# Kernel optimization log

Hardware: AMD Instinct MI355X
Metric: run time of the kernel (lower is better)

## Reference

```python
import jax, jax.numpy as jnp
import numpy as np

B, S, L = 64, 512, 768


def setup_inputs() -> dict:
    key = jax.random.key(0)
    k1, k2 = jax.random.split(key)
    x = jax.random.normal(k1, (B, S, L), dtype=jnp.float32)
    # matches torch uniform_(-0.1, 0.1) init for the probe matrix b
    b = jax.random.uniform(k2, (L, L), minval=-0.1, maxval=0.1, dtype=jnp.float32)
    return {"x": x, "b": b}


def reference(x, b):
    # Original: z[b,i,j,h] = x_i - x_j; h = einsum('gh,bijh', b, z); dist = sum_g h^2
    # Identity: ||b @ (x_i - x_j)||^2 = ||p_i||^2 + ||p_j||^2 - 2 p_i . p_j,  p = x @ b^T
    p = jnp.einsum('gh,bsh->bsg', b, x)          # [B, S, L] projected points
    sq = jnp.sum(p * p, axis=-1)                 # [B, S]  squared norms
    gram = jnp.einsum('bsg,btg->bst', p, p)      # [B, S, S] inner products
    return sq[:, :, None] + sq[:, None, :] - 2.0 * gram  # [B, S, S]
```

## Files before the change

### kernel.cpp

```cpp
#include <hip/hip_runtime.h>
#include <hip/hip_bf16.h>


using bf16x8 = __attribute__((ext_vector_type(8))) __bf16;
using f32x4  = __attribute__((ext_vector_type(4))) float;
using fl4    = __attribute__((ext_vector_type(4))) float;
using u16x4  = __attribute__((ext_vector_type(4))) unsigned short;
using u32x4  = __attribute__((ext_vector_type(4))) unsigned int;

#define NB 64
#define NS 512
#define NL 768

__device__ __forceinline__ unsigned short f2bf(float f) {
  unsigned u = __builtin_bit_cast(unsigned, f);
  u += 0x7FFFu + ((u >> 16) & 1u);
  return (unsigned short)(u >> 16);
}

__device__ __forceinline__ void gload_lds16(const void* g, void* l) {
  __builtin_amdgcn_global_load_lds(
      (const __attribute__((address_space(1))) void*)g,
      (__attribute__((address_space(3))) void*)l, 16, 0, 0);
}

__device__ __forceinline__ bf16x8 cvt_bf8(fl4 a, fl4 b) {
  unsigned r0, r1, r2, r3;
  asm("v_cvt_pk_bf16_f32 %0, %1, %2" : "=v"(r0) : "v"(a[0]), "v"(a[1]));
  asm("v_cvt_pk_bf16_f32 %0, %1, %2" : "=v"(r1) : "v"(a[2]), "v"(a[3]));
  asm("v_cvt_pk_bf16_f32 %0, %1, %2" : "=v"(r2) : "v"(b[0]), "v"(b[1]));
  asm("v_cvt_pk_bf16_f32 %0, %1, %2" : "=v"(r3) : "v"(b[2]), "v"(b[3]));
  u32x4 t = {r0, r1, r2, r3};
  return __builtin_bit_cast(bf16x8, t);
}

#define MEMFENCE asm volatile("" ::: "memory")

__global__ __launch_bounds__(256) void k_cvt_b(const float* __restrict__ b,
                                               unsigned short* __restrict__ bb) {
  const long t = (long)blockIdx.x * 256 + threadIdx.x;
  fl4 v = *(const fl4*)(b + t * 4);
  u16x4 o;
#pragma unroll
  for (int j = 0; j < 4; ++j) o[j] = f2bf(v[j]);
  *(u16x4*)(bb + t * 4) = o;
}

__global__ __launch_bounds__(256) void k_proj(const float* __restrict__ x,
                                              const unsigned short* __restrict__ bb,
                                              unsigned short* __restrict__ p) {
  __shared__ __align__(16) float          smA[3][128 * 32];
  __shared__ __align__(16) unsigned short smB[3][128 * 32];
  const int tid = threadIdx.x;
  const int w = tid >> 6, l = tid & 63;
  const int wg = ((blockIdx.x & 7) * 192) + (blockIdx.x >> 3);
  const int nt = wg % 6, mt = wg / 6;
  const long m0 = (long)mt * 128, n0 = (long)nt * 128;
  const int wr = (w >> 1) * 64, wc = (w & 1) * 64;

  const int arow = tid >> 3;
  const int acol = ((tid & 7) ^ (arow & 7)) * 4;
  const float* gA = x + (m0 + arow) * (long)NL + acol;
  const int brow = tid >> 2;
  const int bcol = ((tid & 3) ^ (brow & 3)) * 8;
  const unsigned short* gB = bb + (n0 + brow) * (long)NL + bcol;

  const int qh = l >> 4, lr = l & 15;
  const int aoff = (wr + lr) * 128;
  const int asw1 = (qh * 32) ^ ((lr & 7) << 4);
  const int asw2 = (qh * 32 + 16) ^ ((lr & 7) << 4);
  const int boff = (wc + lr) * 64 + ((qh ^ (lr & 3)) << 4);

  f32x4 acc[4][4] = {};

#define STAGE_A(k0, buf)                                                     \
  {                                                                          \
    char* d_ = (char*)&smA[buf][0] + w * 1024;                               \
    const float* s_ = gA + (k0);                                             \
    gload_lds16(s_ + 0 * 32 * NL, d_ + 0 * 4096);                            \
    gload_lds16(s_ + 1 * 32 * NL, d_ + 1 * 4096);                            \
    gload_lds16(s_ + 2 * 32 * NL, d_ + 2 * 4096);                            \
    gload_lds16(s_ + 3 * 32 * NL, d_ + 3 * 4096);                            \
  }
#define STAGE_B(k0, buf)                                                     \
  {                                                                          \
    char* d_ = (char*)&smB[buf][0] + w * 1024;                               \
    const unsigned short* s_ = gB + (k0);                                    \
    gload_lds16(s_, d_);                                                     \
    gload_lds16(s_ + 64 * NL, d_ + 4096);                                    \
  }
#define COMPUTE(buf)                                                         \
  {                                                                          \
    const char* A_  = (const char*)&smA[buf][0];                             \
    const char* B_  = (const char*)&smB[buf][0];                             \
    bf16x8 fa[4], fb[4];                                                     \
    _Pragma("unroll")                                                        \
    for (int m = 0; m < 4; ++m) {                                            \
      fl4 a0 = *(const fl4*)(A_ + aoff + m * 2048 + asw1);                   \
      fl4 a1 = *(const fl4*)(A_ + aoff + m * 2048 + asw2);                   \
      fa[m] = cvt_bf8(a0, a1);                                               \
    }                                                                        \
    _Pragma("unroll")                                                        \
    for (int n = 0; n < 4; ++n)                                              \
      fb[n] = *(const bf16x8*)(B_ + boff + n * 1024);                        \
    _Pragma("unroll")                                                        \
    for (int m = 0; m < 4; ++m)                                              \
      _Pragma("unroll")                                                      \
      for (int n = 0; n < 4; ++n)                                            \
        acc[m][n] = __builtin_amdgcn_mfma_f32_16x16x32_bf16(fa[m], fb[n],    \
                                                            acc[m][n], 0, 0, 0); \
  }

  STAGE_A(0, 0)  STAGE_B(0, 0)
  STAGE_A(32, 1) STAGE_B(32, 1)
  int cur = 0, nxt2 = 2;
#pragma unroll 1
  for (int kt = 0; kt < 23; ++kt) {
    asm volatile("s_waitcnt vmcnt(6)" ::: "memory");
    __builtin_amdgcn_s_barrier();
    MEMFENCE;
    if (kt < 22) {
      STAGE_A((kt + 2) * 32, nxt2)
      STAGE_B((kt + 2) * 32, nxt2)
    }
    COMPUTE(cur)
    cur = (cur == 2) ? 0 : cur + 1;
    nxt2 = (nxt2 == 2) ? 0 : nxt2 + 1;
  }
  asm volatile("s_waitcnt vmcnt(0)" ::: "memory");
  __builtin_amdgcn_s_barrier();
  MEMFENCE;
  COMPUTE(cur)
#undef STAGE_A
#undef STAGE_B
#undef COMPUTE

#pragma unroll
  for (int m = 0; m < 4; ++m) {
    const long rbase = m0 + wr + m * 16 + qh * 4;
#pragma unroll
    for (int n = 0; n < 4; ++n) {
      const long col = n0 + wc + n * 16 + lr;
#pragma unroll
      for (int r = 0; r < 4; ++r)
        p[(rbase + r) * NL + col] = f2bf(acc[m][n][r]);
    }
  }
}

__global__ __launch_bounds__(256) void k_sq(const unsigned short* __restrict__ p,
                                            float* __restrict__ sq) {
  const int row = blockIdx.x * 4 + (threadIdx.x >> 6);
  const int l = threadIdx.x & 63;
  const unsigned short* pr = p + (long)row * NL;
  float s = 0.f;
#pragma unroll
  for (int c = 0; c < 3; ++c) {
    u16x4 v = *(const u16x4*)(pr + (c * 64 + l) * 4);
#pragma unroll
    for (int j = 0; j < 4; ++j) {
      float f = __builtin_bit_cast(float, ((unsigned)v[j]) << 16);
      s += f * f;
    }
  }
#pragma unroll
  for (int d = 32; d >= 1; d >>= 1) s += __shfl_xor(s, d, 64);
  if (l == 0) sq[row] = s;
}

__global__ __launch_bounds__(256) void k_gram(const unsigned short* __restrict__ p,
                                              const float* __restrict__ sq,
                                              float* __restrict__ out) {
  __shared__ __align__(16) unsigned short smA[3][128 * 32];
  __shared__ __align__(16) unsigned short smB[3][128 * 32];
  const int tid = threadIdx.x;
  const int w = tid >> 6, l = tid & 63;
  const int wg = ((blockIdx.x & 7) * 128) + (blockIdx.x >> 3);
  const int batch = wg >> 4, tile = wg & 15;
  const int mt = tile >> 2, nt = tile & 3;
  const unsigned short* pb = p + (long)batch * NS * NL;
  const long m0 = (long)mt * 128, n0 = (long)nt * 128;
  const int wr = (w >> 1) * 64, wc = (w & 1) * 64;

  const int srow = tid >> 2;
  const int scol = ((tid & 3) ^ (srow & 3)) * 8;
  const unsigned short* gA = pb + (m0 + srow) * (long)NL + scol;
  const unsigned short* gB = pb + (n0 + srow) * (long)NL + scol;

  const int qh = l >> 4, lr = l & 15;
  const int aoff = (wr + lr) * 64 + ((qh ^ (lr & 3)) << 4);
  const int boff = (wc + lr) * 64 + ((qh ^ (lr & 3)) << 4);

  f32x4 acc[4][4] = {};

#define STAGE2(k0, buf)                                                      \
  {                                                                          \
    char* da_ = (char*)&smA[buf][0] + w * 1024;                              \
    char* db_ = (char*)&smB[buf][0] + w * 1024;                              \
    gload_lds16(gA + (k0), da_);                                             \
    gload_lds16(gA + (k0) + 64 * NL, da_ + 4096);                            \
    gload_lds16(gB + (k0), db_);                                             \
    gload_lds16(gB + (k0) + 64 * NL, db_ + 4096);                            \
  }
#define COMPUTE2(buf)                                                        \
  {                                                                          \
    const char* A_ = (const char*)&smA[buf][0];                              \
    const char* B_ = (const char*)&smB[buf][0];                              \
    bf16x8 fa[4], fb[4];                                                     \
    _Pragma("unroll")                                                        \
    for (int m = 0; m < 4; ++m)                                              \
      fa[m] = *(const bf16x8*)(A_ + aoff + m * 1024);                        \
    _Pragma("unroll")                                                        \
    for (int n = 0; n < 4; ++n)                                              \
      fb[n] = *(const bf16x8*)(B_ + boff + n * 1024);                        \
    _Pragma("unroll")                                                        \
    for (int m = 0; m < 4; ++m)                                              \
      _Pragma("unroll")                                                      \
      for (int n = 0; n < 4; ++n)                                            \
        acc[m][n] = __builtin_amdgcn_mfma_f32_16x16x32_bf16(fa[m], fb[n],    \
                                                            acc[m][n], 0, 0, 0); \
  }

  STAGE2(0, 0)
  STAGE2(32, 1)
  int cur = 0, nxt2 = 2;
#pragma unroll 1
  for (int kt = 0; kt < 23; ++kt) {
    asm volatile("s_waitcnt vmcnt(4)" ::: "memory");
    __builtin_amdgcn_s_barrier();
    MEMFENCE;
    if (kt < 22) STAGE2((kt + 2) * 32, nxt2)
    COMPUTE2(cur)
    cur = (cur == 2) ? 0 : cur + 1;
    nxt2 = (nxt2 == 2) ? 0 : nxt2 + 1;
  }
  asm volatile("s_waitcnt vmcnt(0)" ::: "memory");
  __builtin_amdgcn_s_barrier();
  MEMFENCE;
  COMPUTE2(cur)
#undef STAGE2
#undef COMPUTE2

  const float* sqb = sq + batch * NS;
  float* outb = out + (long)batch * NS * NS;
  float sqc[4];
#pragma unroll
  for (int n = 0; n < 4; ++n) sqc[n] = sqb[n0 + wc + n * 16 + lr];
#pragma unroll
  for (int m = 0; m < 4; ++m) {
#pragma unroll
    for (int r = 0; r < 4; ++r) {
      const long row = m0 + wr + m * 16 + qh * 4 + r;
      const float sr = sqb[row];
#pragma unroll
      for (int n = 0; n < 4; ++n) {
        const long col = n0 + wc + n * 16 + lr;
        outb[row * NS + col] = sr + sqc[n] - 2.0f * acc[m][n][r];
      }
    }
  }
}

extern "C" void kernel_launch(void* const* d_in, const int* in_sizes, int n_in,
                              void* d_out, int out_size, void* d_ws, size_t ws_size,
                              hipStream_t stream) {
  (void)in_sizes; (void)n_in; (void)out_size; (void)ws_size;
  const float* x = (const float*)d_in[0];
  const float* b = (const float*)d_in[1];
  float* out = (float*)d_out;
  char* ws = (char*)d_ws;
  unsigned short* bb = (unsigned short*)ws;
  float* sq          = (float*)(ws + 1179648);
  unsigned short* p  = (unsigned short*)(ws + 1310720);

  k_cvt_b<<<576, 256, 0, stream>>>(b, bb);
  k_proj <<<1536, 256, 0, stream>>>(x, bb, p);
  k_sq   <<<8192, 256, 0, stream>>>(p, sq);
  k_gram <<<1024, 256, 0, stream>>>(p, sq, out);
}
```

Before: 131.8 us.

## Convert x to bf16 once per tile via registers, double-buffer projection LDS

The projection kernel now loads fp32 x tiles into registers, converts each element to bf16 once, and writes bf16 into a padded, swizzled LDS buffer. Previously the fp32 data went straight to LDS via global_load_lds and was converted after every fragment read. The pipeline also shrinks from three LDS stages to two, with a full vmcnt(0) wait and a barrier each iteration. The LDS swizzle for B (and the gram kernel's operands) changes to XOR with (row>>1)&3 to reduce bank conflicts. This halves LDS footprint and traffic for A, but it loses the async direct-to-LDS copy and the deeper prefetch, so more global latency may be exposed.

```diff
diff --git a/kernel.cpp b/kernel.cpp
--- a/kernel.cpp
+++ b/kernel.cpp
@@ -24,16 +24,6 @@
       (__attribute__((address_space(3))) void*)l, 16, 0, 0);
 }
 
-__device__ __forceinline__ bf16x8 cvt_bf8(fl4 a, fl4 b) {
-  unsigned r0, r1, r2, r3;
-  asm("v_cvt_pk_bf16_f32 %0, %1, %2" : "=v"(r0) : "v"(a[0]), "v"(a[1]));
-  asm("v_cvt_pk_bf16_f32 %0, %1, %2" : "=v"(r1) : "v"(a[2]), "v"(a[3]));
-  asm("v_cvt_pk_bf16_f32 %0, %1, %2" : "=v"(r2) : "v"(b[0]), "v"(b[1]));
-  asm("v_cvt_pk_bf16_f32 %0, %1, %2" : "=v"(r3) : "v"(b[2]), "v"(b[3]));
-  u32x4 t = {r0, r1, r2, r3};
-  return __builtin_bit_cast(bf16x8, t);
-}
-
 #define MEMFENCE asm volatile("" ::: "memory")
 
 __global__ __launch_bounds__(256) void k_cvt_b(const float* __restrict__ b,
@@ -49,8 +39,8 @@
 __global__ __launch_bounds__(256) void k_proj(const float* __restrict__ x,
                                               const unsigned short* __restrict__ bb,
                                               unsigned short* __restrict__ p) {
-  __shared__ __align__(16) float          smA[3][128 * 32];
-  __shared__ __align__(16) unsigned short smB[3][128 * 32];
+  __shared__ __align__(16) unsigned short smA[2][128 * 40];
+  __shared__ __align__(16) unsigned short smB[2][128 * 32];
   const int tid = threadIdx.x;
   const int w = tid >> 6, l = tid & 63;
   const int wg = ((blockIdx.x & 7) * 192) + (blockIdx.x >> 3);
@@ -58,51 +48,66 @@
   const long m0 = (long)mt * 128, n0 = (long)nt * 128;
   const int wr = (w >> 1) * 64, wc = (w & 1) * 64;
 
-  const int arow = tid >> 3;
-  const int acol = ((tid & 7) ^ (arow & 7)) * 4;
-  const float* gA = x + (m0 + arow) * (long)NL + acol;
+  const int arow = tid >> 1, ah = tid & 1;
+  const float* gA = x + (m0 + arow) * (long)NL + ah * 16;
+  const int as_ = (arow >> 3) & 3;
+  const int awr0 = arow * 80 + (((2 * ah + 0) ^ as_) << 4);
+  const int awr1 = arow * 80 + (((2 * ah + 1) ^ as_) << 4);
+
   const int brow = tid >> 2;
-  const int bcol = ((tid & 3) ^ (brow & 3)) * 8;
+  const int bcol = ((tid & 3) ^ ((brow >> 1) & 3)) * 8;
   const unsigned short* gB = bb + (n0 + brow) * (long)NL + bcol;
 
   const int qh = l >> 4, lr = l & 15;
-  const int aoff = (wr + lr) * 128;
-  const int asw1 = (qh * 32) ^ ((lr & 7) << 4);
-  const int asw2 = (qh * 32 + 16) ^ ((lr & 7) << 4);
-  const int boff = (wc + lr) * 64 + ((qh ^ (lr & 3)) << 4);
+  int aro[4];
+#pragma unroll
+  for (int m = 0; m < 4; ++m) {
+    const int r = wr + m * 16 + lr;
+    aro[m] = r * 80 + ((qh ^ ((r >> 3) & 3)) << 4);
+  }
+  const int boff = (wc + lr) * 64 + ((qh ^ ((lr >> 1) & 3)) << 4);
 
   f32x4 acc[4][4] = {};
-
-#define STAGE_A(k0, buf)                                                     \
-  {                                                                          \
-    char* d_ = (char*)&smA[buf][0] + w * 1024;                               \
-    const float* s_ = gA + (k0);                                             \
-    gload_lds16(s_ + 0 * 32 * NL, d_ + 0 * 4096);                            \
-    gload_lds16(s_ + 1 * 32 * NL, d_ + 1 * 4096);                            \
-    gload_lds16(s_ + 2 * 32 * NL, d_ + 2 * 4096);                            \
-    gload_lds16(s_ + 3 * 32 * NL, d_ + 3 * 4096);                            \
-  }
-#define STAGE_B(k0, buf)                                                     \
+  fl4 ar0, ar1, ar2, ar3;
+
+#define ISSUE_B(k0, buf)                                                     \
   {                                                                          \
     char* d_ = (char*)&smB[buf][0] + w * 1024;                               \
-    const unsigned short* s_ = gB + (k0);                                    \
-    gload_lds16(s_, d_);                                                     \
-    gload_lds16(s_ + 64 * NL, d_ + 4096);                                    \
+    gload_lds16(gB + (k0), d_);                                              \
+    gload_lds16(gB + (k0) + 64 * NL, d_ + 4096);                             \
+  }
+#define ISSUE_A(k0)                                                          \
+  {                                                                          \
+    ar0 = *(const fl4*)(gA + (k0));                                          \
+    ar1 = *(const fl4*)(gA + (k0) + 4);                                      \
+    ar2 = *(const fl4*)(gA + (k0) + 8);                                      \
+    ar3 = *(const fl4*)(gA + (k0) + 12);                                     \
+  }
+#define WRITE_A(buf)                                                         \
+  {                                                                          \
+    unsigned q0, q1, q2, q3, q4, q5, q6, q7;                                 \
+    asm("v_cvt_pk_bf16_f32 %0, %1, %2" : "=v"(q0) : "v"(ar0[0]), "v"(ar0[1]));\
+    asm("v_cvt_pk_bf16_f32 %0, %1, %2" : "=v"(q1) : "v"(ar0[2]), "v"(ar0[3]));\
+    asm("v_cvt_pk_bf16_f32 %0, %1, %2" : "=v"(q2) : "v"(ar1[0]), "v"(ar1[1]));\
+    asm("v_cvt_pk_bf16_f32 %0, %1, %2" : "=v"(q3) : "v"(ar1[2]), "v"(ar1[3]));\
+    asm("v_cvt_pk_bf16_f32 %0, %1, %2" : "=v"(q4) : "v"(ar2[0]), "v"(ar2[1]));\
+    asm("v_cvt_pk_bf16_f32 %0, %1, %2" : "=v"(q5) : "v"(ar2[2]), "v"(ar2[3]));\
+    asm("v_cvt_pk_bf16_f32 %0, %1, %2" : "=v"(q6) : "v"(ar3[0]), "v"(ar3[1]));\
+    asm("v_cvt_pk_bf16_f32 %0, %1, %2" : "=v"(q7) : "v"(ar3[2]), "v"(ar3[3]));\
+    u32x4 c0 = {q0, q1, q2, q3}, c1 = {q4, q5, q6, q7};                      \
+    char* base_ = (char*)&smA[buf][0];                                       \
+    *(u32x4*)(base_ + awr0) = c0;                                            \
+    *(u32x4*)(base_ + awr1) = c1;                                            \
   }
 #define COMPUTE(buf)                                                         \
   {                                                                          \
-    const char* A_  = (const char*)&smA[buf][0];                             \
-    const char* B_  = (const char*)&smB[buf][0];                             \
+    const char* A_ = (const char*)&smA[buf][0];                              \
+    const char* B_ = (const char*)&smB[buf][0];                              \
     bf16x8 fa[4], fb[4];                                                     \
     _Pragma("unroll")                                                        \
-    for (int m = 0; m < 4; ++m) {                                            \
-      fl4 a0 = *(const fl4*)(A_ + aoff + m * 2048 + asw1);                   \
-      fl4 a1 = *(const fl4*)(A_ + aoff + m * 2048 + asw2);                   \
-      fa[m] = cvt_bf8(a0, a1);                                               \
-    }                                                                        \
-    _Pragma("unroll")                                                        \
-    for (int n = 0; n < 4; ++n)                                              \
-      fb[n] = *(const bf16x8*)(B_ + boff + n * 1024);                        \
+    for (int m = 0; m < 4; ++m) fa[m] = *(const bf16x8*)(A_ + aro[m]);       \
+    _Pragma("unroll")                                                        \
+    for (int n = 0; n < 4; ++n) fb[n] = *(const bf16x8*)(B_ + boff + n * 1024);\
     _Pragma("unroll")                                                        \
     for (int m = 0; m < 4; ++m)                                              \
       _Pragma("unroll")                                                      \
@@ -111,28 +116,33 @@
                                                             acc[m][n], 0, 0, 0); \
   }
 
-  STAGE_A(0, 0)  STAGE_B(0, 0)
-  STAGE_A(32, 1) STAGE_B(32, 1)
-  int cur = 0, nxt2 = 2;
-#pragma unroll 1
-  for (int kt = 0; kt < 23; ++kt) {
-    asm volatile("s_waitcnt vmcnt(6)" ::: "memory");
-    __builtin_amdgcn_s_barrier();
-    MEMFENCE;
-    if (kt < 22) {
-      STAGE_A((kt + 2) * 32, nxt2)
-      STAGE_B((kt + 2) * 32, nxt2)
-    }
-    COMPUTE(cur)
-    cur = (cur == 2) ? 0 : cur + 1;
-    nxt2 = (nxt2 == 2) ? 0 : nxt2 + 1;
-  }
+  ISSUE_B(0, 0)
+  ISSUE_A(0)
   asm volatile("s_waitcnt vmcnt(0)" ::: "memory");
+  WRITE_A(0)
+  asm volatile("s_waitcnt lgkmcnt(0)" ::: "memory");
   __builtin_amdgcn_s_barrier();
   MEMFENCE;
-  COMPUTE(cur)
-#undef STAGE_A
-#undef STAGE_B
+  int cur = 0;
+#pragma unroll 1
+  for (int kt = 0; kt < 24; ++kt) {
+    if (kt < 23) {
+      ISSUE_B((kt + 1) * 32, cur ^ 1)
+      ISSUE_A((kt + 1) * 32)
+    }
+    COMPUTE(cur)
+    if (kt < 23) {
+      asm volatile("s_waitcnt vmcnt(0)" ::: "memory");
+      WRITE_A(cur ^ 1)
+      asm volatile("s_waitcnt lgkmcnt(0)" ::: "memory");
+      __builtin_amdgcn_s_barrier();
+      MEMFENCE;
+      cur ^= 1;
+    }
+  }
+#undef ISSUE_B
+#undef ISSUE_A
+#undef WRITE_A
 #undef COMPUTE
 
 #pragma unroll
@@ -183,13 +193,13 @@
   const int wr = (w >> 1) * 64, wc = (w & 1) * 64;
 
   const int srow = tid >> 2;
-  const int scol = ((tid & 3) ^ (srow & 3)) * 8;
+  const int scol = ((tid & 3) ^ ((srow >> 1) & 3)) * 8;
   const unsigned short* gA = pb + (m0 + srow) * (long)NL + scol;
   const unsigned short* gB = pb + (n0 + srow) * (long)NL + scol;
 
   const int qh = l >> 4, lr = l & 15;
-  const int aoff = (wr + lr) * 64 + ((qh ^ (lr & 3)) << 4);
-  const int boff = (wc + lr) * 64 + ((qh ^ (lr & 3)) << 4);
+  const int aoff = (wr + lr) * 64 + ((qh ^ ((lr >> 1) & 3)) << 4);
+  const int boff = (wc + lr) * 64 + ((qh ^ ((lr >> 1) & 3)) << 4);
 
   f32x4 acc[4][4] = {};
 
```

Result: faster. 120.2 us (-8.8%).

## Pre-convert x to bf16 and widen projection and gram tiles to 128x256

Applied to the files above, without the earlier changes.

Adds a separate pass that converts x to bf16 in workspace, so the projection GEMM streams bf16 for both operands instead of loading fp32 and converting inside the inner loop. Both GEMM kernels move from 128x128 to 128x256 tiles, with 4x8 MFMA accumulators per wave, a new LDS swizzle and launch bounds of 2 blocks. The larger tiles aim to raise operand reuse and cut global and LDS traffic per FLOP. In exchange, the extra pass reads the full fp32 x and writes about 50MB of bf16 through memory, and register pressure and per-block LDS rise while block counts halve.

```diff
diff --git a/kernel.cpp b/kernel.cpp
--- a/kernel.cpp
+++ b/kernel.cpp
@@ -6,7 +6,6 @@
 using f32x4  = __attribute__((ext_vector_type(4))) float;
 using fl4    = __attribute__((ext_vector_type(4))) float;
 using u16x4  = __attribute__((ext_vector_type(4))) unsigned short;
-using u32x4  = __attribute__((ext_vector_type(4))) unsigned int;
 
 #define NB 64
 #define NS 512
@@ -22,16 +21,6 @@
   __builtin_amdgcn_global_load_lds(
       (const __attribute__((address_space(1))) void*)g,
       (__attribute__((address_space(3))) void*)l, 16, 0, 0);
-}
-
-__device__ __forceinline__ bf16x8 cvt_bf8(fl4 a, fl4 b) {
-  unsigned r0, r1, r2, r3;
-  asm("v_cvt_pk_bf16_f32 %0, %1, %2" : "=v"(r0) : "v"(a[0]), "v"(a[1]));
-  asm("v_cvt_pk_bf16_f32 %0, %1, %2" : "=v"(r1) : "v"(a[2]), "v"(a[3]));
-  asm("v_cvt_pk_bf16_f32 %0, %1, %2" : "=v"(r2) : "v"(b[0]), "v"(b[1]));
-  asm("v_cvt_pk_bf16_f32 %0, %1, %2" : "=v"(r3) : "v"(b[2]), "v"(b[3]));
-  u32x4 t = {r0, r1, r2, r3};
-  return __builtin_bit_cast(bf16x8, t);
 }
 
 #define MEMFENCE asm volatile("" ::: "memory")
@@ -46,100 +35,99 @@
   *(u16x4*)(bb + t * 4) = o;
 }
 
-__global__ __launch_bounds__(256) void k_proj(const float* __restrict__ x,
-                                              const unsigned short* __restrict__ bb,
-                                              unsigned short* __restrict__ p) {
-  __shared__ __align__(16) float          smA[3][128 * 32];
-  __shared__ __align__(16) unsigned short smB[3][128 * 32];
+__global__ __launch_bounds__(256) void k_cvt_x(const float* __restrict__ x,
+                                               unsigned short* __restrict__ xb) {
+  const long n4 = (long)NB * NS * NL / 4;
+  const long stride = (long)gridDim.x * 256;
+  for (long i = (long)blockIdx.x * 256 + threadIdx.x; i < n4; i += stride) {
+    fl4 v = *(const fl4*)(x + i * 4);
+    u16x4 o;
+#pragma unroll
+    for (int j = 0; j < 4; ++j) o[j] = f2bf(v[j]);
+    *(u16x4*)(xb + i * 4) = o;
+  }
+}
+
+__global__ __launch_bounds__(256, 2) void k_projb(
+    const unsigned short* __restrict__ xb,
+    const unsigned short* __restrict__ bb,
+    unsigned short* __restrict__ p) {
+  __shared__ __align__(16) unsigned short smA[3][128 * 32];
+  __shared__ __align__(16) unsigned short smB[3][256 * 32];
   const int tid = threadIdx.x;
   const int w = tid >> 6, l = tid & 63;
-  const int wg = ((blockIdx.x & 7) * 192) + (blockIdx.x >> 3);
-  const int nt = wg % 6, mt = wg / 6;
-  const long m0 = (long)mt * 128, n0 = (long)nt * 128;
-  const int wr = (w >> 1) * 64, wc = (w & 1) * 64;
-
-  const int arow = tid >> 3;
-  const int acol = ((tid & 7) ^ (arow & 7)) * 4;
-  const float* gA = x + (m0 + arow) * (long)NL + acol;
-  const int brow = tid >> 2;
-  const int bcol = ((tid & 3) ^ (brow & 3)) * 8;
-  const unsigned short* gB = bb + (n0 + brow) * (long)NL + bcol;
+  const int wg = ((blockIdx.x & 7) * 96) + (blockIdx.x >> 3);
+  const int nt = wg % 3, mt = wg / 3;
+  const long m0 = (long)mt * 128, n0 = (long)nt * 256;
+  const int wr = (w >> 1) * 64, wc = (w & 1) * 128;
+
+  const int srow = tid >> 2;
+  const int scol = ((tid & 3) ^ ((srow >> 1) & 3)) * 8;
+  const unsigned short* gA = xb + (m0 + srow) * (long)NL + scol;
+  const unsigned short* gB = bb + (n0 + srow) * (long)NL + scol;
 
   const int qh = l >> 4, lr = l & 15;
-  const int aoff = (wr + lr) * 128;
-  const int asw1 = (qh * 32) ^ ((lr & 7) << 4);
-  const int asw2 = (qh * 32 + 16) ^ ((lr & 7) << 4);
-  const int boff = (wc + lr) * 64 + ((qh ^ (lr & 3)) << 4);
-
-  f32x4 acc[4][4] = {};
-
-#define STAGE_A(k0, buf)                                                     \
-  {                                                                          \
-    char* d_ = (char*)&smA[buf][0] + w * 1024;                               \
-    const float* s_ = gA + (k0);                                             \
-    gload_lds16(s_ + 0 * 32 * NL, d_ + 0 * 4096);                            \
-    gload_lds16(s_ + 1 * 32 * NL, d_ + 1 * 4096);                            \
-    gload_lds16(s_ + 2 * 32 * NL, d_ + 2 * 4096);                            \
-    gload_lds16(s_ + 3 * 32 * NL, d_ + 3 * 4096);                            \
-  }
-#define STAGE_B(k0, buf)                                                     \
-  {                                                                          \
-    char* d_ = (char*)&smB[buf][0] + w * 1024;                               \
-    const unsigned short* s_ = gB + (k0);                                    \
-    gload_lds16(s_, d_);                                                     \
-    gload_lds16(s_ + 64 * NL, d_ + 4096);                                    \
-  }
-#define COMPUTE(buf)                                                         \
-  {                                                                          \
-    const char* A_  = (const char*)&smA[buf][0];                             \
-    const char* B_  = (const char*)&smB[buf][0];                             \
-    bf16x8 fa[4], fb[4];                                                     \
-    _Pragma("unroll")                                                        \
-    for (int m = 0; m < 4; ++m) {                                            \
-      fl4 a0 = *(const fl4*)(A_ + aoff + m * 2048 + asw1);                   \
-      fl4 a1 = *(const fl4*)(A_ + aoff + m * 2048 + asw2);                   \
-      fa[m] = cvt_bf8(a0, a1);                                               \
-    }                                                                        \
-    _Pragma("unroll")                                                        \
-    for (int n = 0; n < 4; ++n)                                              \
+  const int swz = ((qh ^ ((lr >> 1) & 3)) << 4);
+  const int aoff = (wr + lr) * 64 + swz;
+  const int boff = (wc + lr) * 64 + swz;
+
+  f32x4 acc[4][8] = {};
+
+#define STAGEP(k0, buf)                                                      \
+  {                                                                          \
+    char* da_ = (char*)&smA[buf][0] + w * 1024;                              \
+    char* db_ = (char*)&smB[buf][0] + w * 1024;                              \
+    gload_lds16(gA + (k0), da_);                                             \
+    gload_lds16(gA + (k0) + 64 * NL, da_ + 4096);                            \
+    gload_lds16(gB + (k0), db_);                                             \
+    gload_lds16(gB + (k0) + 64 * NL, db_ + 4096);                            \
+    gload_lds16(gB + (k0) + 128 * NL, db_ + 8192);                           \
+    gload_lds16(gB + (k0) + 192 * NL, db_ + 12288);                          \
+  }
+#define COMPUTEP(buf)                                                        \
+  {                                                                          \
+    const char* A_ = (const char*)&smA[buf][0];                              \
+    const char* B_ = (const char*)&smB[buf][0];                              \
+    bf16x8 fa[4], fb[8];                                                     \
+    _Pragma("unroll")                                                        \
+    for (int m = 0; m < 4; ++m)                                              \
+      fa[m] = *(const bf16x8*)(A_ + aoff + m * 1024);                        \
+    _Pragma("unroll")                                                        \
+    for (int n = 0; n < 8; ++n)                                              \
       fb[n] = *(const bf16x8*)(B_ + boff + n * 1024);                        \
     _Pragma("unroll")                                                        \
     for (int m = 0; m < 4; ++m)                                              \
       _Pragma("unroll")                                                      \
-      for (int n = 0; n < 4; ++n)                                            \
+      for (int n = 0; n < 8; ++n)                                            \
         acc[m][n] = __builtin_amdgcn_mfma_f32_16x16x32_bf16(fa[m], fb[n],    \
                                                             acc[m][n], 0, 0, 0); \
   }
 
-  STAGE_A(0, 0)  STAGE_B(0, 0)
-  STAGE_A(32, 1) STAGE_B(32, 1)
+  STAGEP(0, 0)
+  STAGEP(32, 1)
   int cur = 0, nxt2 = 2;
 #pragma unroll 1
   for (int kt = 0; kt < 23; ++kt) {
     asm volatile("s_waitcnt vmcnt(6)" ::: "memory");
     __builtin_amdgcn_s_barrier();
     MEMFENCE;
-    if (kt < 22) {
-      STAGE_A((kt + 2) * 32, nxt2)
-      STAGE_B((kt + 2) * 32, nxt2)
-    }
-    COMPUTE(cur)
+    if (kt < 22) STAGEP((kt + 2) * 32, nxt2)
+    COMPUTEP(cur)
     cur = (cur == 2) ? 0 : cur + 1;
     nxt2 = (nxt2 == 2) ? 0 : nxt2 + 1;
   }
   asm volatile("s_waitcnt vmcnt(0)" ::: "memory");
   __builtin_amdgcn_s_barrier();
   MEMFENCE;
-  COMPUTE(cur)
-#undef STAGE_A
-#undef STAGE_B
-#undef COMPUTE
+  COMPUTEP(cur)
+#undef STAGEP
+#undef COMPUTEP
 
 #pragma unroll
   for (int m = 0; m < 4; ++m) {
     const long rbase = m0 + wr + m * 16 + qh * 4;
 #pragma unroll
-    for (int n = 0; n < 4; ++n) {
+    for (int n = 0; n < 8; ++n) {
       const long col = n0 + wc + n * 16 + lr;
 #pragma unroll
       for (int r = 0; r < 4; ++r)
@@ -168,32 +156,34 @@
   if (l == 0) sq[row] = s;
 }
 
-__global__ __launch_bounds__(256) void k_gram(const unsigned short* __restrict__ p,
-                                              const float* __restrict__ sq,
-                                              float* __restrict__ out) {
+__global__ __launch_bounds__(256, 2) void k_gram(
+    const unsigned short* __restrict__ p,
+    const float* __restrict__ sq,
+    float* __restrict__ out) {
   __shared__ __align__(16) unsigned short smA[3][128 * 32];
-  __shared__ __align__(16) unsigned short smB[3][128 * 32];
+  __shared__ __align__(16) unsigned short smB[3][256 * 32];
   const int tid = threadIdx.x;
   const int w = tid >> 6, l = tid & 63;
-  const int wg = ((blockIdx.x & 7) * 128) + (blockIdx.x >> 3);
-  const int batch = wg >> 4, tile = wg & 15;
-  const int mt = tile >> 2, nt = tile & 3;
+  const int wg = ((blockIdx.x & 7) * 64) + (blockIdx.x >> 3);
+  const int batch = wg >> 3, tile = wg & 7;
+  const int mt = tile >> 1, nt = tile & 1;
   const unsigned short* pb = p + (long)batch * NS * NL;
-  const long m0 = (long)mt * 128, n0 = (long)nt * 128;
-  const int wr = (w >> 1) * 64, wc = (w & 1) * 64;
+  const long m0 = (long)mt * 128, n0 = (long)nt * 256;
+  const int wr = (w >> 1) * 64, wc = (w & 1) * 128;
 
   const int srow = tid >> 2;
-  const int scol = ((tid & 3) ^ (srow & 3)) * 8;
+  const int scol = ((tid & 3) ^ ((srow >> 1) & 3)) * 8;
   const unsigned short* gA = pb + (m0 + srow) * (long)NL + scol;
   const unsigned short* gB = pb + (n0 + srow) * (long)NL + scol;
 
   const int qh = l >> 4, lr = l & 15;
-  const int aoff = (wr + lr) * 64 + ((qh ^ (lr & 3)) << 4);
-  const int boff = (wc + lr) * 64 + ((qh ^ (lr & 3)) << 4);
-
-  f32x4 acc[4][4] = {};
-
-#define STAGE2(k0, buf)                                                      \
+  const int swz = ((qh ^ ((lr >> 1) & 3)) << 4);
+  const int aoff = (wr + lr) * 64 + swz;
+  const int boff = (wc + lr) * 64 + swz;
+
+  f32x4 acc[4][8] = {};
+
+#define STAGEG(k0, buf)                                                      \
   {                                                                          \
     char* da_ = (char*)&smA[buf][0] + w * 1024;                              \
     char* db_ = (char*)&smB[buf][0] + w * 1024;                              \
@@ -201,51 +191,53 @@
     gload_lds16(gA + (k0) + 64 * NL, da_ + 4096);                            \
     gload_lds16(gB + (k0), db_);                                             \
     gload_lds16(gB + (k0) + 64 * NL, db_ + 4096);                            \
-  }
-#define COMPUTE2(buf)                                                        \
+    gload_lds16(gB + (k0) + 128 * NL, db_ + 8192);                           \
+    gload_lds16(gB + (k0) + 192 * NL, db_ + 12288);                          \
+  }
+#define COMPUTEG(buf)                                                        \
   {                                                                          \
     const char* A_ = (const char*)&smA[buf][0];                              \
     const char* B_ = (const char*)&smB[buf][0];                              \
-    bf16x8 fa[4], fb[4];                                                     \
+    bf16x8 fa[4], fb[8];                                                     \
     _Pragma("unroll")                                                        \
     for (int m = 0; m < 4; ++m)                                              \
       fa[m] = *(const bf16x8*)(A_ + aoff + m * 1024);                        \
     _Pragma("unroll")                                                        \
-    for (int n = 0; n < 4; ++n)                                              \
+    for (int n = 0; n < 8; ++n)                                              \
       fb[n] = *(const bf16x8*)(B_ + boff + n * 1024);                        \
     _Pragma("unroll")                                                        \
     for (int m = 0; m < 4; ++m)                                              \
       _Pragma("unroll")                                                      \
-      for (int n = 0; n < 4; ++n)                                            \
+      for (int n = 0; n < 8; ++n)                                            \
         acc[m][n] = __builtin_amdgcn_mfma_f32_16x16x32_bf16(fa[m], fb[n],    \
                                                             acc[m][n], 0, 0, 0); \
   }
 
-  STAGE2(0, 0)
-  STAGE2(32, 1)
+  STAGEG(0, 0)
+  STAGEG(32, 1)
   int cur = 0, nxt2 = 2;
 #pragma unroll 1
   for (int kt = 0; kt < 23; ++kt) {
-    asm volatile("s_waitcnt vmcnt(4)" ::: "memory");
+    asm volatile("s_waitcnt vmcnt(6)" ::: "memory");
     __builtin_amdgcn_s_barrier();
     MEMFENCE;
-    if (kt < 22) STAGE2((kt + 2) * 32, nxt2)
-    COMPUTE2(cur)
+    if (kt < 22) STAGEG((kt + 2) * 32, nxt2)
+    COMPUTEG(cur)
     cur = (cur == 2) ? 0 : cur + 1;
     nxt2 = (nxt2 == 2) ? 0 : nxt2 + 1;
   }
   asm volatile("s_waitcnt vmcnt(0)" ::: "memory");
   __builtin_amdgcn_s_barrier();
   MEMFENCE;
-  COMPUTE2(cur)
-#undef STAGE2
-#undef COMPUTE2
+  COMPUTEG(cur)
+#undef STAGEG
+#undef COMPUTEG
 
   const float* sqb = sq + batch * NS;
   float* outb = out + (long)batch * NS * NS;
-  float sqc[4];
-#pragma unroll
-  for (int n = 0; n < 4; ++n) sqc[n] = sqb[n0 + wc + n * 16 + lr];
+  float sqc[8];
+#pragma unroll
+  for (int n = 0; n < 8; ++n) sqc[n] = sqb[n0 + wc + n * 16 + lr];
 #pragma unroll
   for (int m = 0; m < 4; ++m) {
 #pragma unroll
@@ -253,7 +245,7 @@
       const long row = m0 + wr + m * 16 + qh * 4 + r;
       const float sr = sqb[row];
 #pragma unroll
-      for (int n = 0; n < 4; ++n) {
+      for (int n = 0; n < 8; ++n) {
         const long col = n0 + wc + n * 16 + lr;
         outb[row * NS + col] = sr + sqc[n] - 2.0f * acc[m][n][r];
       }
@@ -272,9 +264,11 @@
   unsigned short* bb = (unsigned short*)ws;
   float* sq          = (float*)(ws + 1179648);
   unsigned short* p  = (unsigned short*)(ws + 1310720);
+  unsigned short* xb = (unsigned short*)(ws + 51642368);
 
   k_cvt_b<<<576, 256, 0, stream>>>(b, bb);
-  k_proj <<<1536, 256, 0, stream>>>(x, bb, p);
+  k_cvt_x<<<2048, 256, 0, stream>>>(x, xb);
+  k_projb<<<768, 256, 0, stream>>>(xb, bb, p);
   k_sq   <<<8192, 256, 0, stream>>>(p, sq);
-  k_gram <<<1024, 256, 0, stream>>>(p, sq, out);
-}
+  k_gram <<<512, 256, 0, stream>>>(p, sq, out);
+}
```

Measured after the change: 133.6 us. About the same (+1.4%).
